# Kernel tuning notes

Hardware: AMD Instinct MI355X
Metric: run time of the kernel (lower is better)

Reference implementation:

```python
import jax, jax.numpy as jnp
import numpy as np

N_NODES = 50000
N_EDGES = 600000
EMBED_DIM = 128


def setup_inputs() -> dict:
    key = jax.random.key(0)
    k1, k2 = jax.random.split(key)
    x = jax.random.normal(k1, (N_NODES, EMBED_DIM), dtype=jnp.float32)
    edge_index = jax.random.randint(k2, (2, N_EDGES), 0, N_NODES, dtype=jnp.int64)
    bias = jnp.zeros((EMBED_DIM,), dtype=jnp.float32)
    return {"x": x, "edge_index": edge_index, "bias": bias}


def reference(x, edge_index, bias):
    # init_embedding is Identity (disable_init_embedding=True)
    init_embeds = x
    n = x.shape[0]
    # add_self_loops
    loops = jnp.arange(n, dtype=edge_index.dtype)
    row = jnp.concatenate([edge_index[0], loops])  # source nodes
    col = jnp.concatenate([edge_index[1], loops])  # destination nodes
    # degree of destination nodes
    deg = jax.ops.segment_sum(jnp.ones_like(col, dtype=x.dtype), col, num_segments=n)
    deg_inv_sqrt = jnp.where(deg > 0, jax.lax.rsqrt(jnp.maximum(deg, 1e-20)), 0.0)
    # symmetric GCN normalization per edge
    norm = deg_inv_sqrt[row] * deg_inv_sqrt[col]  # [E+N]
    # message: gather source features, scale, scatter-add into destinations
    msg = norm[:, None] * x[row]  # [E+N, D]
    out = jax.ops.segment_sum(msg, col, num_segments=n) + bias
    return (out, init_embeds)
```

## Files before the change

### kernel.cpp

```cpp
#include <hip/hip_runtime.h>

#define D 128
#define B 256
#define WMAX 64
#define SPILL_MAX 8192
#define NPART 8

typedef float vfloat4 __attribute__((ext_vector_type(4)));


__device__ __forceinline__ unsigned short f2bf(float f) {
    unsigned u = __float_as_uint(f);
    u = u + 0x7FFFu + ((u >> 16) & 1u);
    return (unsigned short)(u >> 16);
}

__device__ __forceinline__ vfloat4 bf2f4(uint2 v) {
    vfloat4 r;
    r.x = __uint_as_float(v.x << 16);
    r.y = __uint_as_float(v.x & 0xffff0000u);
    r.z = __uint_as_float(v.y << 16);
    r.w = __uint_as_float(v.y & 0xffff0000u);
    return r;
}

__global__ void k_prep(const float* __restrict__ x, float* __restrict__ out2,
                       uint2* __restrict__ xb, int* __restrict__ cursor,
                       int* __restrict__ spillCnt, int n) {
    int gid = blockIdx.x * blockDim.x + threadIdx.x;
    if (gid == 0) *spillCnt = 0;
    if (gid < n) cursor[gid] = 0;
    if (gid >= n * 32) return;
    vfloat4 xv = reinterpret_cast<const vfloat4*>(x)[gid];
    __builtin_nontemporal_store(xv, reinterpret_cast<vfloat4*>(out2) + gid);
    uint2 b;
    b.x = (unsigned)f2bf(xv.x) | ((unsigned)f2bf(xv.y) << 16);
    b.y = (unsigned)f2bf(xv.z) | ((unsigned)f2bf(xv.w) << 16);
    xb[gid] = b;
}

__global__ void k_place_ell(const int* __restrict__ row, const int* __restrict__ col,
                            int* __restrict__ cursor, int* __restrict__ ssrc,
                            int2* __restrict__ spill, int* __restrict__ spillCnt,
                            int e, int n) {
    int p  = blockIdx.x & (NPART - 1);
    int bg = blockIdx.x >> 3;
    int tg = bg * blockDim.x + threadIdx.x;
    int T  = (gridDim.x >> 3) * blockDim.x;
    int lo = (int)((long long)n * p / NPART);
    int hi = (int)((long long)n * (p + 1) / NPART);

    for (int i = tg; i < e; i += T) {
        int c = col[i];
        if (c < lo || c >= hi) continue;
        int r = row[i];
        int pos = atomicAdd(&cursor[c], 1);
        if (pos < WMAX) {
            ssrc[c * WMAX + pos] = r;
        } else {
            int s = atomicAdd(spillCnt, 1);
            if (s < SPILL_MAX) spill[s] = make_int2(r, c);
        }
    }
}

__global__ void k_agg_ell(const uint2* __restrict__ xb, const float* __restrict__ bias,
                          const int* __restrict__ cursor, const int* __restrict__ ssrc,
                          const int2* __restrict__ spill, const int* __restrict__ spillCnt,
                          float* __restrict__ out, int n) {
    int bpg = (gridDim.x + NPART - 1) >> 3;
    int node_block = (blockIdx.x & (NPART - 1)) * bpg + (blockIdx.x >> 3);
    int node = node_block * 8 + (threadIdx.x >> 5);
    if (node >= n) return;
    int q = threadIdx.x & 31;

    int cnt = cursor[node];
    int m   = min(cnt, WMAX);
    const int* sp = ssrc + node * WMAX;

    vfloat4 a0 = {0.f, 0.f, 0.f, 0.f};
    vfloat4 a1 = a0, a2 = a0, a3 = a0;

    int j = 0;
    for (; j + 4 <= m; j += 4) {
        int r0 = sp[j + 0], r1 = sp[j + 1], r2 = sp[j + 2], r3 = sp[j + 3];
        uint2 v0 = xb[(size_t)r0 * 32 + q];
        uint2 v1 = xb[(size_t)r1 * 32 + q];
        uint2 v2 = xb[(size_t)r2 * 32 + q];
        uint2 v3 = xb[(size_t)r3 * 32 + q];
        float w0 = rsqrtf((float)cursor[r0] + 1.0f);
        float w1 = rsqrtf((float)cursor[r1] + 1.0f);
        float w2 = rsqrtf((float)cursor[r2] + 1.0f);
        float w3 = rsqrtf((float)cursor[r3] + 1.0f);
        a0 += w0 * bf2f4(v0);
        a1 += w1 * bf2f4(v1);
        a2 += w2 * bf2f4(v2);
        a3 += w3 * bf2f4(v3);
    }
    for (; j < m; ++j) {
        int r = sp[j];
        uint2 v = xb[(size_t)r * 32 + q];
        float w = rsqrtf((float)cursor[r] + 1.0f);
        a0 += w * bf2f4(v);
    }

    if (cnt > WMAX) {
        int sc = min(*spillCnt, SPILL_MAX);
        for (int s = 0; s < sc; ++s) {
            int2 pr = spill[s];
            if (pr.y == node) {
                float w = rsqrtf((float)cursor[pr.x] + 1.0f);
                a0 += w * bf2f4(xb[(size_t)pr.x * 32 + q]);
            }
        }
    }

    float dc = rsqrtf((float)cnt + 1.0f);
    vfloat4 xc = bf2f4(xb[(size_t)node * 32 + q]);
    vfloat4 bv = reinterpret_cast<const vfloat4*>(bias)[q];
    vfloat4 ov = bv + dc * (a0 + a1 + a2 + a3 + dc * xc);

    __builtin_nontemporal_store(ov, reinterpret_cast<vfloat4*>(out) + (size_t)node * 32 + q);
}


__global__ void k_zero(int* __restrict__ degInt, int n) {
    int i = blockIdx.x * blockDim.x + threadIdx.x;
    if (i < n) degInt[i] = 0;
}

__global__ void k_count(const int* __restrict__ col, int* __restrict__ degInt, int e) {
    int i = blockIdx.x * blockDim.x + threadIdx.x;
    if (i < e) atomicAdd(&degInt[col[i]], 1);
}

__global__ void k_scan1(const int* __restrict__ degInt, int* __restrict__ off,
                        int* __restrict__ bsum, int n) {
    __shared__ int sm[B];
    int i = blockIdx.x * B + threadIdx.x;
    int v = (i < n) ? degInt[i] : 0;
    sm[threadIdx.x] = v;
    __syncthreads();
    for (int s = 1; s < B; s <<= 1) {
        int t = (threadIdx.x >= (unsigned)s) ? sm[threadIdx.x - s] : 0;
        __syncthreads();
        sm[threadIdx.x] += t;
        __syncthreads();
    }
    if (i < n) off[i] = sm[threadIdx.x] - v;
    if (threadIdx.x == B - 1) bsum[blockIdx.x] = sm[B - 1];
}

__global__ void k_scan2(int* __restrict__ bsum, int nb) {
    __shared__ int sm[B];
    int v = (threadIdx.x < (unsigned)nb) ? bsum[threadIdx.x] : 0;
    sm[threadIdx.x] = v;
    __syncthreads();
    for (int s = 1; s < B; s <<= 1) {
        int t = (threadIdx.x >= (unsigned)s) ? sm[threadIdx.x - s] : 0;
        __syncthreads();
        sm[threadIdx.x] += t;
        __syncthreads();
    }
    if (threadIdx.x < (unsigned)nb) bsum[threadIdx.x] = sm[threadIdx.x] - v;
}

__global__ void k_scan3(int* __restrict__ off, const int* __restrict__ bsum,
                        const int* __restrict__ degInt, float* __restrict__ dis,
                        int* __restrict__ cursor, int n, int e) {
    int i = blockIdx.x * B + threadIdx.x;
    if (i < n) {
        int o = off[i] + bsum[blockIdx.x];
        off[i] = o;
        cursor[i] = o;
        dis[i] = rsqrtf((float)degInt[i] + 1.0f);
    }
    if (i == 0) off[n] = e;
}

__global__ void k_place_pairs(const int* __restrict__ row, const int* __restrict__ col,
                              const float* __restrict__ dis, int* __restrict__ cursor,
                              int2* __restrict__ pairs, int e) {
    int i = blockIdx.x * blockDim.x + threadIdx.x;
    if (i >= e) return;
    int r = row[i];
    int c = col[i];
    float w = dis[r];
    int pos = atomicAdd(&cursor[c], 1);
    pairs[pos] = make_int2(r, __float_as_int(w));
}

__global__ void k_aggregate_pairs(const float* __restrict__ x, const float* __restrict__ bias,
                                  const float* __restrict__ dis, const int* __restrict__ off,
                                  const int2* __restrict__ pairs, float* __restrict__ out,
                                  float* __restrict__ out2, int n) {
    int gid = blockIdx.x * blockDim.x + threadIdx.x;
    if (gid >= n * 32) return;
    int node = gid >> 5;
    int q    = gid & 31;
    const vfloat4* x4 = reinterpret_cast<const vfloat4*>(x);
    int j   = off[node];
    int end = off[node + 1];
    vfloat4 a0 = {0.f, 0.f, 0.f, 0.f};
    vfloat4 a1 = a0, a2 = a0, a3 = a0;
    for (; j + 4 <= end; j += 4) {
        int2 p0 = pairs[j + 0];
        int2 p1 = pairs[j + 1];
        int2 p2 = pairs[j + 2];
        int2 p3 = pairs[j + 3];
        vfloat4 v0 = x4[(size_t)p0.x * 32 + q];
        vfloat4 v1 = x4[(size_t)p1.x * 32 + q];
        vfloat4 v2 = x4[(size_t)p2.x * 32 + q];
        vfloat4 v3 = x4[(size_t)p3.x * 32 + q];
        a0 += __int_as_float(p0.y) * v0;
        a1 += __int_as_float(p1.y) * v1;
        a2 += __int_as_float(p2.y) * v2;
        a3 += __int_as_float(p3.y) * v3;
    }
    for (; j < end; ++j) {
        int2 p = pairs[j];
        a0 += __int_as_float(p.y) * x4[(size_t)p.x * 32 + q];
    }
    float dc = dis[node];
    vfloat4 xc = x4[(size_t)node * 32 + q];
    vfloat4 bv = reinterpret_cast<const vfloat4*>(bias)[q];
    vfloat4 ov = bv + dc * (a0 + a1 + a2 + a3 + dc * xc);
    __builtin_nontemporal_store(ov, reinterpret_cast<vfloat4*>(out)  + (size_t)node * 32 + q);
    __builtin_nontemporal_store(xc, reinterpret_cast<vfloat4*>(out2) + (size_t)node * 32 + q);
}


extern "C" void kernel_launch(void* const* d_in, const int* in_sizes, int n_in,
                              void* d_out, int out_size, void* d_ws, size_t ws_size,
                              hipStream_t stream) {
    const float* x    = (const float*)d_in[0];
    const int*   idx  = (const int*)d_in[1];
    const float* bias = (const float*)d_in[2];

    const int n = in_sizes[0] / D;
    const int e = in_sizes[1] / 2;

    const int* row = idx;
    const int* col = idx + e;

    float* out  = (float*)d_out;
    float* out2 = (float*)d_out + (size_t)n * D;

    const int nbN = (n + B - 1) / B;
    const int nbE = (e + B - 1) / B;
    const int aggB = (n * 32 + B - 1) / B;

    char* p0 = (char*)d_ws;
    int*  cursor  = (int*)p0;                        p0 += (size_t)n * 4;
    int*  spillCnt= (int*)p0;                        p0 += 16;
    int2* spill   = (int2*)p0;                       p0 += (size_t)SPILL_MAX * 8;
    p0 = (char*)(((uintptr_t)p0 + 15) & ~(uintptr_t)15);
    uint2* xb     = (uint2*)p0;                      p0 += (size_t)n * 32 * 8;
    int*  ssrc    = (int*)p0;                        p0 += (size_t)n * WMAX * 4;
    size_t need_ell = (size_t)(p0 - (char*)d_ws);

    if (ws_size >= need_ell) {
        const int plB = 2048;
        const int bpg  = (n + 8 * NPART - 1) / (8 * NPART);
        const int agB  = bpg * NPART;
        k_prep     <<<aggB, B, 0, stream>>>(x, out2, xb, cursor, spillCnt, n);
        k_place_ell<<<plB,  B, 0, stream>>>(row, col, cursor, ssrc, spill, spillCnt, e, n);
        k_agg_ell  <<<agB,  B, 0, stream>>>(xb, bias, cursor, ssrc, spill, spillCnt, out, n);
        return;
    }

    char* p = (char*)d_ws;
    int*   degInt = (int*)p;            p += (size_t)n * 4;
    int*   cur2   = (int*)p;            p += (size_t)n * 4;
    int*   off    = (int*)p;            p += (size_t)(n + 1) * 4;
    int*   bsum   = (int*)p;            p += 256 * 4;
    float* dis    = (float*)p;          p += (size_t)n * 4;
    p = (char*)(((uintptr_t)p + 15) & ~(uintptr_t)15);
    int2*  pairs  = (int2*)p;

    k_zero <<<nbN, B, 0, stream>>>(degInt, n);
    k_count<<<nbE, B, 0, stream>>>(col, degInt, e);
    k_scan1<<<nbN, B, 0, stream>>>(degInt, off, bsum, n);
    k_scan2<<<1,   B, 0, stream>>>(bsum, nbN);
    k_scan3<<<nbN, B, 0, stream>>>(off, bsum, degInt, dis, cur2, n, e);
    k_place_pairs<<<nbE, B, 0, stream>>>(row, col, dis, cur2, pairs, e);
    k_aggregate_pairs<<<aggB, B, 0, stream>>>(x, bias, dis, off, pairs, out, out2, n);
}
```

Measured before the change: 77.10 us.

## Merge prep and ELL placement into one kernel, align aggregation partitions

Splits cursor zeroing into a small kernel, then runs the edge-placement work and the bf16 conversion/copy of x as two block ranges of a single launch so they overlap. The aggregation kernel now maps its block groups to the same node partitions used during placement, aiming for locality in the cursor and slot arrays. This trades one launch for another and risks placement blocks competing with the bandwidth-heavy conversion blocks.

```diff
diff --git a/kernel.cpp b/kernel.cpp
--- a/kernel.cpp
+++ b/kernel.cpp
@@ -5,6 +5,7 @@
 #define WMAX 64
 #define SPILL_MAX 8192
 #define NPART 8
+#define PLACE_BLOCKS 2048
 
 typedef float vfloat4 __attribute__((ext_vector_type(4)));
 
@@ -15,52 +16,59 @@
     return (unsigned short)(u >> 16);
 }
 
-__device__ __forceinline__ vfloat4 bf2f4(uint2 v) {
+__device__ __forceinline__ vfloat4 bf2f4(unsigned lo, unsigned hi) {
     vfloat4 r;
-    r.x = __uint_as_float(v.x << 16);
-    r.y = __uint_as_float(v.x & 0xffff0000u);
-    r.z = __uint_as_float(v.y << 16);
-    r.w = __uint_as_float(v.y & 0xffff0000u);
+    r.x = __uint_as_float(lo << 16);
+    r.y = __uint_as_float(lo & 0xffff0000u);
+    r.z = __uint_as_float(hi << 16);
+    r.w = __uint_as_float(hi & 0xffff0000u);
     return r;
 }
 
-__global__ void k_prep(const float* __restrict__ x, float* __restrict__ out2,
-                       uint2* __restrict__ xb, int* __restrict__ cursor,
-                       int* __restrict__ spillCnt, int n) {
-    int gid = blockIdx.x * blockDim.x + threadIdx.x;
-    if (gid == 0) *spillCnt = 0;
-    if (gid < n) cursor[gid] = 0;
-    if (gid >= n * 32) return;
-    vfloat4 xv = reinterpret_cast<const vfloat4*>(x)[gid];
-    __builtin_nontemporal_store(xv, reinterpret_cast<vfloat4*>(out2) + gid);
-    uint2 b;
-    b.x = (unsigned)f2bf(xv.x) | ((unsigned)f2bf(xv.y) << 16);
-    b.y = (unsigned)f2bf(xv.z) | ((unsigned)f2bf(xv.w) << 16);
-    xb[gid] = b;
-}
-
-__global__ void k_place_ell(const int* __restrict__ row, const int* __restrict__ col,
-                            int* __restrict__ cursor, int* __restrict__ ssrc,
-                            int2* __restrict__ spill, int* __restrict__ spillCnt,
-                            int e, int n) {
-    int p  = blockIdx.x & (NPART - 1);
-    int bg = blockIdx.x >> 3;
-    int tg = bg * blockDim.x + threadIdx.x;
-    int T  = (gridDim.x >> 3) * blockDim.x;
-    int lo = (int)((long long)n * p / NPART);
-    int hi = (int)((long long)n * (p + 1) / NPART);
-
-    for (int i = tg; i < e; i += T) {
-        int c = col[i];
-        if (c < lo || c >= hi) continue;
-        int r = row[i];
-        int pos = atomicAdd(&cursor[c], 1);
-        if (pos < WMAX) {
-            ssrc[c * WMAX + pos] = r;
-        } else {
-            int s = atomicAdd(spillCnt, 1);
-            if (s < SPILL_MAX) spill[s] = make_int2(r, c);
+__global__ void k_zero2(int* __restrict__ cursor, int* __restrict__ spillCnt, int n) {
+    int i = blockIdx.x * blockDim.x + threadIdx.x;
+    if (i == 0) *spillCnt = 0;
+    if (i < n) cursor[i] = 0;
+}
+
+__global__ void k_mega(const float* __restrict__ x, float* __restrict__ out2,
+                       uint2* __restrict__ xb,
+                       const int* __restrict__ row, const int* __restrict__ col,
+                       int* __restrict__ cursor, int* __restrict__ ssrc,
+                       int2* __restrict__ spill, int* __restrict__ spillCnt,
+                       int e, int n) {
+    int bid = blockIdx.x;
+    int t   = threadIdx.x;
+
+    if (bid < PLACE_BLOCKS) {
+        int p  = bid & (NPART - 1);
+        int bg = bid >> 3;
+        int tg = bg * B + t;
+        int T  = (PLACE_BLOCKS >> 3) * B;
+        int lo = (int)((long long)n * p / NPART);
+        int hi = (int)((long long)n * (p + 1) / NPART);
+
+        for (int i = tg; i < e; i += T) {
+            int c = col[i];
+            if (c < lo || c >= hi) continue;
+            int r = row[i];
+            int pos = atomicAdd(&cursor[c], 1);
+            if (pos < WMAX) {
+                ssrc[c * WMAX + pos] = r;
+            } else {
+                int s = atomicAdd(spillCnt, 1);
+                if (s < SPILL_MAX) spill[s] = make_int2(r, c);
+            }
         }
+    } else {
+        int gid = (bid - PLACE_BLOCKS) * B + t;
+        if (gid >= n * 32) return;
+        vfloat4 xv = reinterpret_cast<const vfloat4*>(x)[gid];
+        __builtin_nontemporal_store(xv, reinterpret_cast<vfloat4*>(out2) + gid);
+        uint2 b;
+        b.x = (unsigned)f2bf(xv.x) | ((unsigned)f2bf(xv.y) << 16);
+        b.y = (unsigned)f2bf(xv.z) | ((unsigned)f2bf(xv.w) << 16);
+        xb[gid] = b;
     }
 }
 
@@ -68,10 +76,12 @@
                           const int* __restrict__ cursor, const int* __restrict__ ssrc,
                           const int2* __restrict__ spill, const int* __restrict__ spillCnt,
                           float* __restrict__ out, int n) {
-    int bpg = (gridDim.x + NPART - 1) >> 3;
-    int node_block = (blockIdx.x & (NPART - 1)) * bpg + (blockIdx.x >> 3);
-    int node = node_block * 8 + (threadIdx.x >> 5);
-    if (node >= n) return;
+    int p  = blockIdx.x & (NPART - 1);
+    int bg = blockIdx.x >> 3;
+    int lo = (int)((long long)n * p / NPART);
+    int hi = (int)((long long)n * (p + 1) / NPART);
+    int node = lo + bg * 8 + (threadIdx.x >> 5);
+    if (node >= hi) return;
     int q = threadIdx.x & 31;
 
     int cnt = cursor[node];
@@ -92,16 +102,16 @@
         float w1 = rsqrtf((float)cursor[r1] + 1.0f);
         float w2 = rsqrtf((float)cursor[r2] + 1.0f);
         float w3 = rsqrtf((float)cursor[r3] + 1.0f);
-        a0 += w0 * bf2f4(v0);
-        a1 += w1 * bf2f4(v1);
-        a2 += w2 * bf2f4(v2);
-        a3 += w3 * bf2f4(v3);
+        a0 += w0 * bf2f4(v0.x, v0.y);
+        a1 += w1 * bf2f4(v1.x, v1.y);
+        a2 += w2 * bf2f4(v2.x, v2.y);
+        a3 += w3 * bf2f4(v3.x, v3.y);
     }
     for (; j < m; ++j) {
         int r = sp[j];
         uint2 v = xb[(size_t)r * 32 + q];
         float w = rsqrtf((float)cursor[r] + 1.0f);
-        a0 += w * bf2f4(v);
+        a0 += w * bf2f4(v.x, v.y);
     }
 
     if (cnt > WMAX) {
@@ -110,13 +120,15 @@
             int2 pr = spill[s];
             if (pr.y == node) {
                 float w = rsqrtf((float)cursor[pr.x] + 1.0f);
-                a0 += w * bf2f4(xb[(size_t)pr.x * 32 + q]);
+                uint2 v = xb[(size_t)pr.x * 32 + q];
+                a0 += w * bf2f4(v.x, v.y);
             }
         }
     }
 
     float dc = rsqrtf((float)cnt + 1.0f);
-    vfloat4 xc = bf2f4(xb[(size_t)node * 32 + q]);
+    uint2 xc2 = xb[(size_t)node * 32 + q];
+    vfloat4 xc = bf2f4(xc2.x, xc2.y);
     vfloat4 bv = reinterpret_cast<const vfloat4*>(bias)[q];
     vfloat4 ov = bv + dc * (a0 + a1 + a2 + a3 + dc * xc);
 
@@ -246,9 +258,9 @@
     float* out  = (float*)d_out;
     float* out2 = (float*)d_out + (size_t)n * D;
 
-    const int nbN = (n + B - 1) / B;
-    const int nbE = (e + B - 1) / B;
-    const int aggB = (n * 32 + B - 1) / B;
+    const int nbN  = (n + B - 1) / B;
+    const int nbE  = (e + B - 1) / B;
+    const int prepB = (n * 32 + B - 1) / B;
 
     char* p0 = (char*)d_ws;
     int*  cursor  = (int*)p0;                        p0 += (size_t)n * 4;
@@ -260,12 +272,20 @@
     size_t need_ell = (size_t)(p0 - (char*)d_ws);
 
     if (ws_size >= need_ell) {
-        const int plB = 2048;
-        const int bpg  = (n + 8 * NPART - 1) / (8 * NPART);
-        const int agB  = bpg * NPART;
-        k_prep     <<<aggB, B, 0, stream>>>(x, out2, xb, cursor, spillCnt, n);
-        k_place_ell<<<plB,  B, 0, stream>>>(row, col, cursor, ssrc, spill, spillCnt, e, n);
-        k_agg_ell  <<<agB,  B, 0, stream>>>(xb, bias, cursor, ssrc, spill, spillCnt, out, n);
+        int maxPart = 0;
+        for (int p = 0; p < NPART; ++p) {
+            int lo = (int)((long long)n * p / NPART);
+            int hi = (int)((long long)n * (p + 1) / NPART);
+            if (hi - lo > maxPart) maxPart = hi - lo;
+        }
+        const int bpg = (maxPart + 7) / 8;
+        const int agB = bpg * NPART;
+        const int megaB = PLACE_BLOCKS + prepB;
+
+        k_zero2  <<<nbN,   B, 0, stream>>>(cursor, spillCnt, n);
+        k_mega   <<<megaB, B, 0, stream>>>(x, out2, xb, row, col, cursor, ssrc,
+                                           spill, spillCnt, e, n);
+        k_agg_ell<<<agB,   B, 0, stream>>>(xb, bias, cursor, ssrc, spill, spillCnt, out, n);
         return;
     }
 
@@ -278,6 +298,7 @@
     p = (char*)(((uintptr_t)p + 15) & ~(uintptr_t)15);
     int2*  pairs  = (int2*)p;
 
+    const int aggB = (n * 32 + B - 1) / B;
     k_zero <<<nbN, B, 0, stream>>>(degInt, n);
     k_count<<<nbE, B, 0, stream>>>(col, degInt, e);
     k_scan1<<<nbN, B, 0, stream>>>(degInt, off, bsum, n);
```

Measured after the change: 78.99 us. 2.4% more time.

## Sort neighbors by source slice in shared memory and use one wavefront per node

Applied to the files above, without the earlier changes.

The ELL aggregation kernel is replaced by one that gives each node a full 64-lane wavefront, with each lane handling one 32-bit bf16 pair. It loads the node's neighbor list once, computes the per-neighbor weights in parallel, and bucket-sorts the neighbors by source-index slice in shared memory. The sort is meant to improve cache locality of the gathered rows across concurrent blocks. The cost is extra block-wide syncs and shared-memory atomics, plus half as many nodes per block and narrower per-lane loads.

```diff
diff --git a/kernel.cpp b/kernel.cpp
--- a/kernel.cpp
+++ b/kernel.cpp
@@ -5,8 +5,10 @@
 #define WMAX 64
 #define SPILL_MAX 8192
 #define NPART 8
+#define NSLICE 4
 
 typedef float vfloat4 __attribute__((ext_vector_type(4)));
+typedef float vfloat2 __attribute__((ext_vector_type(2)));
 
 
 __device__ __forceinline__ unsigned short f2bf(float f) {
@@ -14,15 +16,8 @@
     u = u + 0x7FFFu + ((u >> 16) & 1u);
     return (unsigned short)(u >> 16);
 }
-
-__device__ __forceinline__ vfloat4 bf2f4(uint2 v) {
-    vfloat4 r;
-    r.x = __uint_as_float(v.x << 16);
-    r.y = __uint_as_float(v.x & 0xffff0000u);
-    r.z = __uint_as_float(v.y << 16);
-    r.w = __uint_as_float(v.y & 0xffff0000u);
-    return r;
-}
+__device__ __forceinline__ float bflo(unsigned u) { return __uint_as_float(u << 16); }
+__device__ __forceinline__ float bfhi(unsigned u) { return __uint_as_float(u & 0xffff0000u); }
 
 __global__ void k_prep(const float* __restrict__ x, float* __restrict__ out2,
                        uint2* __restrict__ xb, int* __restrict__ cursor,
@@ -64,63 +59,94 @@
     }
 }
 
-__global__ void k_agg_ell(const uint2* __restrict__ xb, const float* __restrict__ bias,
-                          const int* __restrict__ cursor, const int* __restrict__ ssrc,
-                          const int2* __restrict__ spill, const int* __restrict__ spillCnt,
-                          float* __restrict__ out, int n) {
-    int bpg = (gridDim.x + NPART - 1) >> 3;
-    int node_block = (blockIdx.x & (NPART - 1)) * bpg + (blockIdx.x >> 3);
-    int node = node_block * 8 + (threadIdx.x >> 5);
-    if (node >= n) return;
-    int q = threadIdx.x & 31;
-
-    int cnt = cursor[node];
+__global__ void k_agg_sl(const unsigned* __restrict__ xbu, const float* __restrict__ bias,
+                         const int* __restrict__ cursor, const int* __restrict__ ssrc,
+                         const int2* __restrict__ spill, const int* __restrict__ spillCnt,
+                         float* __restrict__ out, int n) {
+    __shared__ int   s_srt[4][WMAX];
+    __shared__ float s_wsrt[4][WMAX];
+    __shared__ int   s_off[4][NSLICE + 1];
+
+    int p  = blockIdx.x & (NPART - 1);
+    int bg = blockIdx.x >> 3;
+    int lo = (int)((long long)n * p / NPART);
+    int hi = (int)((long long)n * (p + 1) / NPART);
+    int t = threadIdx.x, wid = t >> 6, lane = t & 63;
+    int node = lo + bg * 4 + wid;
+    bool active = (node < hi);
+
+    int cnt = active ? cursor[node] : 0;
     int m   = min(cnt, WMAX);
-    const int* sp = ssrc + node * WMAX;
-
-    vfloat4 a0 = {0.f, 0.f, 0.f, 0.f};
-    vfloat4 a1 = a0, a2 = a0, a3 = a0;
-
-    int j = 0;
-    for (; j + 4 <= m; j += 4) {
-        int r0 = sp[j + 0], r1 = sp[j + 1], r2 = sp[j + 2], r3 = sp[j + 3];
-        uint2 v0 = xb[(size_t)r0 * 32 + q];
-        uint2 v1 = xb[(size_t)r1 * 32 + q];
-        uint2 v2 = xb[(size_t)r2 * 32 + q];
-        uint2 v3 = xb[(size_t)r3 * 32 + q];
-        float w0 = rsqrtf((float)cursor[r0] + 1.0f);
-        float w1 = rsqrtf((float)cursor[r1] + 1.0f);
-        float w2 = rsqrtf((float)cursor[r2] + 1.0f);
-        float w3 = rsqrtf((float)cursor[r3] + 1.0f);
-        a0 += w0 * bf2f4(v0);
-        a1 += w1 * bf2f4(v1);
-        a2 += w2 * bf2f4(v2);
-        a3 += w3 * bf2f4(v3);
-    }
-    for (; j < m; ++j) {
-        int r = sp[j];
-        uint2 v = xb[(size_t)r * 32 + q];
-        float w = rsqrtf((float)cursor[r] + 1.0f);
-        a0 += w * bf2f4(v);
+
+    if (lane <= NSLICE) s_off[wid][lane] = 0;
+    __syncthreads();
+
+    int myslice = 0, mypos = 0, myr = 0;
+    float myw = 0.f;
+    bool have = active && (lane < m);
+    if (have) {
+        myr = ssrc[node * WMAX + lane];
+        myw = rsqrtf((float)cursor[myr] + 1.0f);
+        myslice = (int)(((long long)myr * NSLICE) / n);
+        if (myslice > NSLICE - 1) myslice = NSLICE - 1;
+        mypos = atomicAdd(&s_off[wid][myslice + 1], 1);
+    }
+    __syncthreads();
+    if (lane == 0) {
+        int acc = 0;
+#pragma unroll
+        for (int s2 = 1; s2 <= NSLICE; ++s2) { acc += s_off[wid][s2]; s_off[wid][s2] = acc; }
+    }
+    __syncthreads();
+    if (have) {
+        int wp = s_off[wid][myslice] + mypos;
+        s_srt[wid][wp]  = myr;
+        s_wsrt[wid][wp] = myw;
+    }
+    __syncthreads();
+
+    if (!active) return;
+
+    float aLo = 0.f, aHi = 0.f, bLo = 0.f, bHi = 0.f;
+#pragma unroll
+    for (int s2 = 0; s2 < NSLICE; ++s2) {
+        int j  = s_off[wid][s2];
+        int je = s_off[wid][s2 + 1];
+        for (; j + 2 <= je; j += 2) {
+            int   r0 = s_srt[wid][j],     r1 = s_srt[wid][j + 1];
+            float w0 = s_wsrt[wid][j],    w1 = s_wsrt[wid][j + 1];
+            unsigned u0 = xbu[(size_t)r0 * 64 + lane];
+            unsigned u1 = xbu[(size_t)r1 * 64 + lane];
+            aLo += w0 * bflo(u0);  aHi += w0 * bfhi(u0);
+            bLo += w1 * bflo(u1);  bHi += w1 * bfhi(u1);
+        }
+        if (j < je) {
+            int   r0 = s_srt[wid][j];
+            float w0 = s_wsrt[wid][j];
+            unsigned u0 = xbu[(size_t)r0 * 64 + lane];
+            aLo += w0 * bflo(u0);  aHi += w0 * bfhi(u0);
+        }
     }
 
     if (cnt > WMAX) {
         int sc = min(*spillCnt, SPILL_MAX);
-        for (int s = 0; s < sc; ++s) {
-            int2 pr = spill[s];
+        for (int s2 = 0; s2 < sc; ++s2) {
+            int2 pr = spill[s2];
             if (pr.y == node) {
                 float w = rsqrtf((float)cursor[pr.x] + 1.0f);
-                a0 += w * bf2f4(xb[(size_t)pr.x * 32 + q]);
+                unsigned u = xbu[(size_t)pr.x * 64 + lane];
+                aLo += w * bflo(u);  aHi += w * bfhi(u);
             }
         }
     }
 
     float dc = rsqrtf((float)cnt + 1.0f);
-    vfloat4 xc = bf2f4(xb[(size_t)node * 32 + q]);
-    vfloat4 bv = reinterpret_cast<const vfloat4*>(bias)[q];
-    vfloat4 ov = bv + dc * (a0 + a1 + a2 + a3 + dc * xc);
-
-    __builtin_nontemporal_store(ov, reinterpret_cast<vfloat4*>(out) + (size_t)node * 32 + q);
+    unsigned xc = xbu[(size_t)node * 64 + lane];
+    float2 bv = reinterpret_cast<const float2*>(bias)[lane];
+    vfloat2 ov;
+    ov.x = bv.x + dc * (aLo + bLo + dc * bflo(xc));
+    ov.y = bv.y + dc * (aHi + bHi + dc * bfhi(xc));
+    __builtin_nontemporal_store(ov, reinterpret_cast<vfloat2*>(out) + (size_t)node * 64 + lane);
 }
 
 
@@ -248,7 +274,7 @@
 
     const int nbN = (n + B - 1) / B;
     const int nbE = (e + B - 1) / B;
-    const int aggB = (n * 32 + B - 1) / B;
+    const int prepB = (n * 32 + B - 1) / B;
 
     char* p0 = (char*)d_ws;
     int*  cursor  = (int*)p0;                        p0 += (size_t)n * 4;
@@ -261,11 +287,18 @@
 
     if (ws_size >= need_ell) {
         const int plB = 2048;
-        const int bpg  = (n + 8 * NPART - 1) / (8 * NPART);
-        const int agB  = bpg * NPART;
-        k_prep     <<<aggB, B, 0, stream>>>(x, out2, xb, cursor, spillCnt, n);
-        k_place_ell<<<plB,  B, 0, stream>>>(row, col, cursor, ssrc, spill, spillCnt, e, n);
-        k_agg_ell  <<<agB,  B, 0, stream>>>(xb, bias, cursor, ssrc, spill, spillCnt, out, n);
+        int maxPart = 0;
+        for (int p = 0; p < NPART; ++p) {
+            int lo = (int)((long long)n * p / NPART);
+            int hi = (int)((long long)n * (p + 1) / NPART);
+            if (hi - lo > maxPart) maxPart = hi - lo;
+        }
+        const int bpg = (maxPart + 3) / 4;
+        const int agB = bpg * NPART;
+        k_prep     <<<prepB, B, 0, stream>>>(x, out2, xb, cursor, spillCnt, n);
+        k_place_ell<<<plB,   B, 0, stream>>>(row, col, cursor, ssrc, spill, spillCnt, e, n);
+        k_agg_sl   <<<agB,   B, 0, stream>>>(reinterpret_cast<const unsigned*>(xb), bias,
+                                             cursor, ssrc, spill, spillCnt, out, n);
         return;
     }
 
@@ -278,6 +311,7 @@
     p = (char*)(((uintptr_t)p + 15) & ~(uintptr_t)15);
     int2*  pairs  = (int2*)p;
 
+    const int aggB = (n * 32 + B - 1) / B;
     k_zero <<<nbN, B, 0, stream>>>(degInt, n);
     k_count<<<nbE, B, 0, stream>>>(col, degInt, e);
     k_scan1<<<nbN, B, 0, stream>>>(degInt, off, bsum, n);
```

Result: slower. 84.42 us (+9.5%).
